# Optimization experiments

Measured on AMD Instinct MI355X. Metric: run time of the kernel, lower is better.

The kernel has to match this reference:

```python
import jax, jax.numpy as jnp
import numpy as np

B, N, C = 8, 2048, 512


def setup_inputs() -> dict:
    key = jax.random.key(0)
    ks = jax.random.split(key, 8)
    s = 1.0 / np.sqrt(C)
    return {
        "x": jax.random.normal(ks[0], (B, N, C), dtype=jnp.float32),
        "Wq": jax.random.normal(ks[1], (C, C), dtype=jnp.float32) * s,
        "Wk": jax.random.normal(ks[2], (C, C), dtype=jnp.float32) * s,
        "Wv": jax.random.normal(ks[3], (C, C), dtype=jnp.float32) * s,
        "W1": jax.random.normal(ks[4], (C, C), dtype=jnp.float32) * s,
        "W2": jax.random.normal(ks[5], (C, C), dtype=jnp.float32) * s,
        "gamma": jax.random.normal(ks[6], (1,), dtype=jnp.float32),
        "beta_p": jax.random.normal(ks[7], (1,), dtype=jnp.float32),
    }


def reference(x, Wq, Wk, Wv, W1, W2, gamma, beta_p):
    # torch.nn.Linear(bias=False): y = x @ W.T  with W of shape [out, in]
    q = jnp.einsum('bnc,dc->bnd', x, Wq)  # [B,N,C]
    k = jnp.einsum('bnc,dc->bnd', x, Wk)
    v = jnp.einsum('bnc,dc->bnd', x, Wv)
    # scores[b,i,j] = q_i . k_j ; softmax over dim=1 (the i axis), as in source
    scores = jnp.einsum('bic,bjc->bij', q, k)        # [B,N,N]
    attn = jax.nn.softmax(scores, axis=1)            # normalize over i
    # bmm(v^T, attn): out[b,c,j] = sum_i v[b,i,c] * attn[b,i,j]; permuted back -> [B,N,C]
    att_out = jnp.einsum('bic,bij->bjc', v, attn)    # [B,N,C]
    o = gamma * att_out + x                          # gamma-scaled residual
    h = jax.nn.relu(jnp.einsum('bnc,dc->bnd', o, W1))
    o = beta_p * jnp.einsum('bnc,dc->bnd', h, W2) + o
    return o
```

## Files before the change

kernel.cpp:

```cpp
#include <hip/hip_runtime.h>
#include <stdint.h>

#define DEVINL __device__ __forceinline__

typedef short short8_t __attribute__((ext_vector_type(8)));
typedef float f32x4_t  __attribute__((ext_vector_type(4)));
typedef _Float16 half8_t __attribute__((ext_vector_type(8)));
typedef unsigned short u16;

static constexpr int  Bn = 8;
static constexpr int  Nn = 2048;
static constexpr int  Cn = 512;
static constexpr int  Mn = Bn * Nn;
static constexpr long NC = (long)Nn * Cn;
static constexpr long NNe = (long)Nn * Nn;
static constexpr long CC = (long)Cn * Cn;
static constexpr long MC = (long)Mn * Cn;

DEVINL u16 f32_to_f16(float f) {
  _Float16 h = (_Float16)f;
  u16 r; __builtin_memcpy(&r, &h, 2);
  return r;
}

DEVINL void mfma_f16(f32x4_t& d, short8_t a, short8_t b) {
  asm("v_mfma_f32_16x16x32_f16 %0, %1, %2, %0" : "+v"(d) : "v"(a), "v"(b));
}

#define GLOAD_LDS16(G, L)                                                      \
  __builtin_amdgcn_global_load_lds(                                            \
      (const __attribute__((address_space(1))) void*)(G),                      \
      (__attribute__((address_space(3))) void*)(L), 16, 0, 0)

__global__ __launch_bounds__(256) void conv_x_kernel(const float* __restrict__ src,
                                                     u16* __restrict__ f16, int n4) {
  int i = blockIdx.x * 256 + threadIdx.x;
  if (i >= n4) return;
  float4 v = ((const float4*)src)[i];
  ((ushort4*)f16)[i] = make_ushort4(f32_to_f16(v.x), f32_to_f16(v.y),
                                    f32_to_f16(v.z), f32_to_f16(v.w));
}

struct W5 { const float* p[5]; };
__global__ __launch_bounds__(256) void conv_w_kernel(W5 ws, u16* __restrict__ f16,
                                                     int n4each) {
  const int w = blockIdx.y;
  const int i = blockIdx.x * 256 + threadIdx.x;
  if (i >= n4each) return;
  float4 v = ((const float4*)ws.p[w])[i];
  ((ushort4*)f16)[(long)w * (CC / 4) + i] =
      make_ushort4(f32_to_f16(v.x), f32_to_f16(v.y), f32_to_f16(v.z), f32_to_f16(v.w));
}

enum { EPI_QKV = 0, EPI_SF16 = 2, EPI_PV = 3, EPI_RELU = 4, EPI_FFN2 = 5 };

template <int BN, int EPI, int SW>
__global__ __launch_bounds__(512, 2) void gemm_k(
    const u16* Ah, const u16* Bh,
    int K, int outld, void* out0, void* out1,
    const float* aux, const float* scal,
    int batch0, long azStride, long bzStride, long ozStride) {
  constexpr int BM = 256, BK = 64;
  constexpr int FN = BN / 64;
  constexpr int ABYTES = BM * BK * 2;
  constexpr int BBYTES = BN * BK * 2;
  constexpr int PB = ABYTES + BBYTES;

  __shared__ __align__(1024) char lds[2 * PB];

  const int tid = threadIdx.x;
  const int l   = tid & 63;
  const int wid = tid >> 6;

  int bx, byy, bz;
  {
    const int gx = gridDim.x, gy = gridDim.y, gz = gridDim.z;
    const int lid = blockIdx.x + gx * (blockIdx.y + gy * blockIdx.z);
    if (SW == 0) {
      const int c = lid & 7, s = lid >> 3;
      const int nyz = gy * gz;
      const int xi = s / nyz, yz = s - xi * nyz;
      bx = c + 8 * xi; byy = yz % gy; bz = yz / gy;
    } else if (SW == 1) {
      bz = lid & 7;
      const int s = lid >> 3;
      byy = s % gy; bx = s / gy;
    } else {
      bx = blockIdx.x; byy = blockIdx.y; bz = blockIdx.z;
    }
  }

  const int batch = batch0 + bz;
  const int brow  = bx * BM;
  const int bcol  = byy * BN;

  Ah += (long)bz * azStride;
  Bh += (long)bz * bzStride;

  const int wrL  = (wid >> 2) * 128;
  const int wcL  = (wid & 3) * (BN / 4);
  const int rsel = l & 15;

  f32x4_t acc[8][FN];
  const f32x4_t zero = {0.f, 0.f, 0.f, 0.f};
#pragma unroll
  for (int m = 0; m < 8; ++m)
#pragma unroll
    for (int n = 0; n < FN; ++n) acc[m][n] = zero;

  const int cb = ((l & 7) ^ ((l >> 3) & 7)) * 8;
  auto stageA = [&](int k0, char* dst) {
#pragma unroll
    for (int j = 0; j < 4; ++j) {
      const int rr = (wid * 4 + j) * 8 + (l >> 3);
      GLOAD_LDS16(Ah + (long)(brow + rr) * K + (k0 + cb), dst + (wid * 4 + j) * 1024);
    }
  };
  auto stageB = [&](int k0, char* dst) {
#pragma unroll
    for (int j = 0; j < FN; ++j) {
      const int rr = (wid * FN + j) * 8 + (l >> 3);
      GLOAD_LDS16(Bh + (long)(bcol + rr) * K + (k0 + cb), dst + (wid * FN + j) * 1024);
    }
  };
  auto stageAll = [&](int k0, char* b) { stageA(k0, b); stageB(k0, b + ABYTES); };

  auto rdA = [&](const char* bufA, int m, int ks) -> short8_t {
    const int r = wrL + m * 16 + rsel;
    const int s = ks * 4 + (l >> 4);
    return *(const short8_t*)(bufA + r * 128 + ((s ^ (r & 7)) << 4));
  };
  auto rdB = [&](const char* bufB, int n, int ks) -> short8_t {
    const int r = wcL + n * 16 + rsel;
    const int s = ks * 4 + (l >> 4);
    return *(const short8_t*)(bufB + r * 128 + ((s ^ (r & 7)) << 4));
  };

  const int NT = K >> 6;
  stageAll(0, lds);
  for (int kt = 0; kt < NT; ++kt) {
    const char* bb = lds + (kt & 1) * PB;
    if (kt + 1 < NT) {
      stageAll((kt + 1) << 6, lds + ((kt + 1) & 1) * PB);
      __builtin_amdgcn_sched_barrier(0);
      if constexpr (FN == 2)
        asm volatile("s_waitcnt vmcnt(6)" ::: "memory");
      else
        asm volatile("s_waitcnt vmcnt(8)" ::: "memory");
    } else {
      __builtin_amdgcn_sched_barrier(0);
      asm volatile("s_waitcnt vmcnt(0)" ::: "memory");
    }
    __builtin_amdgcn_sched_barrier(0);
    __builtin_amdgcn_s_barrier();
    asm volatile("" ::: "memory");
    __builtin_amdgcn_sched_barrier(0);

    short8_t bf[FN][2];
#pragma unroll
    for (int n = 0; n < FN; ++n)
#pragma unroll
      for (int ks = 0; ks < 2; ++ks) bf[n][ks] = rdB(bb + ABYTES, n, ks);

    __builtin_amdgcn_s_setprio(1);
#pragma unroll
    for (int p = 0; p < 4; ++p) {
      short8_t a[2][2];
#pragma unroll
      for (int mm = 0; mm < 2; ++mm)
#pragma unroll
        for (int ks = 0; ks < 2; ++ks) a[mm][ks] = rdA(bb, 2 * p + mm, ks);
#pragma unroll
      for (int mm = 0; mm < 2; ++mm)
#pragma unroll
        for (int n = 0; n < FN; ++n)
#pragma unroll
          for (int ks = 0; ks < 2; ++ks)
            mfma_f16(acc[2 * p + mm][n], a[mm][ks], bf[n][ks]);
    }
    __builtin_amdgcn_s_setprio(0);

    __builtin_amdgcn_sched_barrier(0);
    asm volatile("" ::: "memory");
    __builtin_amdgcn_s_barrier();
    __builtin_amdgcn_sched_barrier(0);
  }

  const float sc0 = scal ? scal[0] : 0.0f;
  const int crow = (l >> 4) * 4;
  const int ccol = l & 15;

  if (EPI == EPI_QKV && (bcol >> 9) == 2) {
    constexpr int TP2 = 264;
    u16* t = (u16*)lds;
#pragma unroll
    for (int m = 0; m < 8; ++m)
#pragma unroll
      for (int n = 0; n < FN; ++n) {
        ushort4 pk = make_ushort4(f32_to_f16(acc[m][n][0]), f32_to_f16(acc[m][n][1]),
                                  f32_to_f16(acc[m][n][2]), f32_to_f16(acc[m][n][3]));
        *(ushort4*)&t[(wcL + n * 16 + ccol) * TP2 + (wrL + m * 16 + crow)] = pk;
      }
    __syncthreads();
    const int colq = tid >> 2, qf = tid & 3;
    const long b = brow >> 11;
    const int cv = bcol - 1024 + colq;
    u16* dst = (u16*)out1 + ((b * Cn + cv) * (long)Nn + (brow & 2047) + qf * 64);
    const u16* srcT = &t[colq * TP2 + qf * 64];
#pragma unroll
    for (int i = 0; i < 8; ++i)
      ((uint4*)dst)[i] = *(const uint4*)(srcT + i * 8);
    return;
  }

#pragma unroll
  for (int m = 0; m < 8; ++m)
#pragma unroll
    for (int n = 0; n < FN; ++n)
#pragma unroll
      for (int j = 0; j < 4; ++j) {
        const int r = brow + wrL + m * 16 + crow + j;
        const int c = bcol + wcL + n * 16 + ccol;
        const float v = acc[m][n][j];
        if (EPI == EPI_QKV) {
          ((u16*)out0)[(long)(c >> 9) * MC + (long)r * Cn + (c & 511)] = f32_to_f16(v);
        } else if (EPI == EPI_SF16) {
          ((u16*)out0 + (long)bz * ozStride)[(long)r * outld + c] = f32_to_f16(v);
        } else if (EPI == EPI_PV) {
          const long gi = ((long)batch * Nn + r) * Cn + c;
          const float val = sc0 * v + aux[gi];
          ((float*)out0)[gi] = val;
          ((u16*)out1)[gi] = f32_to_f16(val);
        } else if (EPI == EPI_RELU) {
          const float val = v > 0.f ? v : 0.f;
          ((u16*)out0)[(long)r * outld + c] = f32_to_f16(val);
        } else {
          const long gi = (long)r * Cn + c;
          ((float*)out0)[gi] = sc0 * v + aux[gi];
        }
      }
}

__global__ __launch_bounds__(256) void softmax_k(const u16* sc, u16* attn) {
  const long base = (long)blockIdx.y * NNe + (long)blockIdx.x * Nn;
  const int tid = threadIdx.x;
  const int l = tid & 63, wid = tid >> 6;
  half8_t v = ((const half8_t*)(sc + base))[tid];
  float f[8];
#pragma unroll
  for (int i = 0; i < 8; ++i) f[i] = (float)v[i];
  float mx = f[0];
#pragma unroll
  for (int i = 1; i < 8; ++i) mx = fmaxf(mx, f[i]);
#pragma unroll
  for (int o = 32; o > 0; o >>= 1) mx = fmaxf(mx, __shfl_xor(mx, o));
  __shared__ float red[8];
  if (l == 0) red[wid] = mx;
  __syncthreads();
  mx = fmaxf(fmaxf(red[0], red[1]), fmaxf(red[2], red[3]));
  float p[8];
  float s = 0.f;
#pragma unroll
  for (int i = 0; i < 8; ++i) { p[i] = __expf(f[i] - mx); s += p[i]; }
#pragma unroll
  for (int o = 32; o > 0; o >>= 1) s += __shfl_xor(s, o);
  if (l == 0) red[4 + wid] = s;
  __syncthreads();
  s = red[4] + red[5] + red[6] + red[7];
  const float inv = 1.0f / s;
  __align__(16) u16 o8[8];
#pragma unroll
  for (int i = 0; i < 8; ++i) o8[i] = f32_to_f16(p[i] * inv);
  ((uint4*)(attn + base))[tid] = *(const uint4*)o8;
}

extern "C" void kernel_launch(void* const* d_in, const int* in_sizes, int n_in,
                              void* d_out, int out_size, void* d_ws, size_t ws_size,
                              hipStream_t stream) {
  const float* x  = (const float*)d_in[0];
  const float* gamma = (const float*)d_in[6];
  const float* beta  = (const float*)d_in[7];
  float* out = (float*)d_out;

  char* ws = (char*)d_ws;
  size_t off = 0;
  auto alloc = [&](size_t bytes) {
    char* p = ws + off;
    off += (bytes + 1023) & ~(size_t)1023;
    return p;
  };
  u16* x16  = (u16*)alloc((size_t)MC * 2);
  u16* w16A = (u16*)alloc((size_t)5 * CC * 2);
  u16* qk16 = (u16*)alloc((size_t)2 * MC * 2);
  u16* vT   = (u16*)alloc((size_t)MC * 2);
  u16* o16  = (u16*)alloc((size_t)MC * 2);
  u16* h16  = (u16*)alloc((size_t)MC * 2);
  const size_t baseOff = off;

  int zAtt = 8;
  while (zAtt > 1 &&
         baseOff + (size_t)zAtt * (NNe * 2 + 1024 + NNe * 2 + 1024) > ws_size)
    zAtt >>= 1;
  u16* scoresT = (u16*)alloc((size_t)zAtt * NNe * 2);
  u16* attnT   = (u16*)alloc((size_t)zAtt * NNe * 2);
  u16* q16 = qk16;
  u16* k16 = qk16 + (size_t)MC;

  conv_x_kernel<<<dim3(MC / 4 / 256), 256, 0, stream>>>(x, x16, MC / 4);
  W5 w5 = {{(const float*)d_in[1], (const float*)d_in[2], (const float*)d_in[3],
            (const float*)d_in[4], (const float*)d_in[5]}};
  conv_w_kernel<<<dim3(CC / 4 / 256, 5), 256, 0, stream>>>(w5, w16A, CC / 4);

  gemm_k<128,EPI_QKV,0><<<dim3(Mn/256, 1536/128, 1), 512, 0, stream>>>(
      x16, w16A, Cn, Cn, qk16, vT, nullptr, nullptr, 0, 0, 0, 0);

  if (zAtt == 8) {
    gemm_k<256,EPI_SF16,1><<<dim3(Nn/256, Nn/256, 8), 512, 0, stream>>>(
        k16, q16, Cn, Nn, scoresT, nullptr, nullptr, nullptr, 0, NC, NC, NNe);
    softmax_k<<<dim3(Nn, 8), 256, 0, stream>>>(scoresT, attnT);
    gemm_k<128,EPI_PV,1><<<dim3(Nn/256, Cn/128, 8), 512, 0, stream>>>(
        attnT, vT, Nn, Cn, out, o16, x, gamma, 0, NNe, NC, 0);
  } else {
    for (int b0 = 0; b0 < Bn; b0 += zAtt) {
      gemm_k<256,EPI_SF16,2><<<dim3(Nn/256, Nn/256, zAtt), 512, 0, stream>>>(
          k16 + (long)b0 * NC, q16 + (long)b0 * NC,
          Cn, Nn, scoresT, nullptr, nullptr, nullptr, b0, NC, NC, NNe);
      softmax_k<<<dim3(Nn, zAtt), 256, 0, stream>>>(scoresT, attnT);
      gemm_k<128,EPI_PV,2><<<dim3(Nn/256, Cn/128, zAtt), 512, 0, stream>>>(
          attnT, vT + (long)b0 * NC, Nn, Cn, out, o16, x, gamma,
          b0, NNe, NC, 0);
    }
  }

  gemm_k<128,EPI_RELU,0><<<dim3(Mn/256, Cn/128, 1), 512, 0, stream>>>(
      o16, w16A + 3 * CC, Cn, Cn, h16, nullptr, nullptr, nullptr, 0, 0, 0, 0);
  gemm_k<128,EPI_FFN2,0><<<dim3(Mn/256, Cn/128, 1), 512, 0, stream>>>(
      h16, w16A + 4 * CC, Cn, Cn, out, nullptr, out, beta, 0, 0, 0, 0);
}
```

Baseline: 232.0 us.

## Rework GEMM warp tiling to 4 N-fragments and widen QKV tile to 256

Each wave now always computes 4 N-fragments, with the M-fragment count varying by tile width (8 for BN=256, 4 for BN=128). BN=128 kernels use a 4x2 wave grid of 64x64 subtiles instead of 2x4 of 128x32. The QKV projection launches with BN=256 tiles, and its transposed V epilogue runs in two passes through LDS. The aim is better operand reuse per A fragment and fewer QKV blocks, at the cost of more accumulator registers and an extra LDS pass with barriers in the V epilogue.

```diff
diff --git a/kernel.cpp b/kernel.cpp
--- a/kernel.cpp
+++ b/kernel.cpp
@@ -61,7 +61,9 @@
     const float* aux, const float* scal,
     int batch0, long azStride, long bzStride, long ozStride) {
   constexpr int BM = 256, BK = 64;
-  constexpr int FN = BN / 64;
+  constexpr int FM = (BN == 256) ? 8 : 4;
+  constexpr int FN = 4;
+  constexpr int BISS = BN / 64;
   constexpr int ABYTES = BM * BK * 2;
   constexpr int BBYTES = BN * BK * 2;
   constexpr int PB = ABYTES + BBYTES;
@@ -97,14 +99,14 @@
   Ah += (long)bz * azStride;
   Bh += (long)bz * bzStride;
 
-  const int wrL  = (wid >> 2) * 128;
-  const int wcL  = (wid & 3) * (BN / 4);
+  const int wrL  = (BN == 256) ? (wid >> 2) * 128 : (wid >> 1) * 64;
+  const int wcL  = (BN == 256) ? (wid & 3) * 64   : (wid & 1) * 64;
   const int rsel = l & 15;
 
-  f32x4_t acc[8][FN];
+  f32x4_t acc[FM][FN];
   const f32x4_t zero = {0.f, 0.f, 0.f, 0.f};
 #pragma unroll
-  for (int m = 0; m < 8; ++m)
+  for (int m = 0; m < FM; ++m)
 #pragma unroll
     for (int n = 0; n < FN; ++n) acc[m][n] = zero;
 
@@ -118,9 +120,9 @@
   };
   auto stageB = [&](int k0, char* dst) {
 #pragma unroll
-    for (int j = 0; j < FN; ++j) {
-      const int rr = (wid * FN + j) * 8 + (l >> 3);
-      GLOAD_LDS16(Bh + (long)(bcol + rr) * K + (k0 + cb), dst + (wid * FN + j) * 1024);
+    for (int j = 0; j < BISS; ++j) {
+      const int rr = (wid * BISS + j) * 8 + (l >> 3);
+      GLOAD_LDS16(Bh + (long)(bcol + rr) * K + (k0 + cb), dst + (wid * BISS + j) * 1024);
     }
   };
   auto stageAll = [&](int k0, char* b) { stageA(k0, b); stageB(k0, b + ABYTES); };
@@ -143,10 +145,10 @@
     if (kt + 1 < NT) {
       stageAll((kt + 1) << 6, lds + ((kt + 1) & 1) * PB);
       __builtin_amdgcn_sched_barrier(0);
-      if constexpr (FN == 2)
+      if constexpr (BN == 256)
+        asm volatile("s_waitcnt vmcnt(8)" ::: "memory");
+      else
         asm volatile("s_waitcnt vmcnt(6)" ::: "memory");
-      else
-        asm volatile("s_waitcnt vmcnt(8)" ::: "memory");
     } else {
       __builtin_amdgcn_sched_barrier(0);
       asm volatile("s_waitcnt vmcnt(0)" ::: "memory");
@@ -164,19 +166,14 @@
 
     __builtin_amdgcn_s_setprio(1);
 #pragma unroll
-    for (int p = 0; p < 4; ++p) {
-      short8_t a[2][2];
-#pragma unroll
-      for (int mm = 0; mm < 2; ++mm)
-#pragma unroll
-        for (int ks = 0; ks < 2; ++ks) a[mm][ks] = rdA(bb, 2 * p + mm, ks);
-#pragma unroll
-      for (int mm = 0; mm < 2; ++mm)
-#pragma unroll
-        for (int n = 0; n < FN; ++n)
-#pragma unroll
-          for (int ks = 0; ks < 2; ++ks)
-            mfma_f16(acc[2 * p + mm][n], a[mm][ks], bf[n][ks]);
+    for (int m = 0; m < FM; ++m) {
+      short8_t a0 = rdA(bb, m, 0);
+      short8_t a1 = rdA(bb, m, 1);
+#pragma unroll
+      for (int n = 0; n < FN; ++n) {
+        mfma_f16(acc[m][n], a0, bf[n][0]);
+        mfma_f16(acc[m][n], a1, bf[n][1]);
+      }
     }
     __builtin_amdgcn_s_setprio(0);
 
@@ -190,31 +187,39 @@
   const int crow = (l >> 4) * 4;
   const int ccol = l & 15;
 
-  if (EPI == EPI_QKV && (bcol >> 9) == 2) {
-    constexpr int TP2 = 264;
+  if (EPI == EPI_QKV && bcol >= 1024) {
+    constexpr int TPV = 264;
     u16* t = (u16*)lds;
-#pragma unroll
-    for (int m = 0; m < 8; ++m)
-#pragma unroll
-      for (int n = 0; n < FN; ++n) {
-        ushort4 pk = make_ushort4(f32_to_f16(acc[m][n][0]), f32_to_f16(acc[m][n][1]),
-                                  f32_to_f16(acc[m][n][2]), f32_to_f16(acc[m][n][3]));
-        *(ushort4*)&t[(wcL + n * 16 + ccol) * TP2 + (wrL + m * 16 + crow)] = pk;
+    const long b = brow >> 11;
+#pragma unroll
+    for (int pass = 0; pass < 2; ++pass) {
+      __syncthreads();
+      if (((wid & 3) >> 1) == pass) {
+        const int clBase = wcL - pass * 128;
+#pragma unroll
+        for (int m = 0; m < FM; ++m)
+#pragma unroll
+          for (int n = 0; n < FN; ++n) {
+            ushort4 pk = make_ushort4(
+                f32_to_f16(acc[m][n][0]), f32_to_f16(acc[m][n][1]),
+                f32_to_f16(acc[m][n][2]), f32_to_f16(acc[m][n][3]));
+            *(ushort4*)&t[(clBase + n * 16 + ccol) * TPV + (wrL + m * 16 + crow)] = pk;
+          }
       }
-    __syncthreads();
-    const int colq = tid >> 2, qf = tid & 3;
-    const long b = brow >> 11;
-    const int cv = bcol - 1024 + colq;
-    u16* dst = (u16*)out1 + ((b * Cn + cv) * (long)Nn + (brow & 2047) + qf * 64);
-    const u16* srcT = &t[colq * TP2 + qf * 64];
-#pragma unroll
-    for (int i = 0; i < 8; ++i)
-      ((uint4*)dst)[i] = *(const uint4*)(srcT + i * 8);
+      __syncthreads();
+      const int colq = tid >> 2, qf = tid & 3;
+      const int cv = bcol - 1024 + pass * 128 + colq;
+      u16* dst = (u16*)out1 + ((b * Cn + cv) * (long)Nn + (brow & 2047) + qf * 64);
+      const u16* srcT = &t[colq * TPV + qf * 64];
+#pragma unroll
+      for (int i = 0; i < 8; ++i)
+        ((uint4*)dst)[i] = *(const uint4*)(srcT + i * 8);
+    }
     return;
   }
 
 #pragma unroll
-  for (int m = 0; m < 8; ++m)
+  for (int m = 0; m < FM; ++m)
 #pragma unroll
     for (int n = 0; n < FN; ++n)
 #pragma unroll
@@ -311,7 +316,7 @@
             (const float*)d_in[4], (const float*)d_in[5]}};
   conv_w_kernel<<<dim3(CC / 4 / 256, 5), 256, 0, stream>>>(w5, w16A, CC / 4);
 
-  gemm_k<128,EPI_QKV,0><<<dim3(Mn/256, 1536/128, 1), 512, 0, stream>>>(
+  gemm_k<256,EPI_QKV,0><<<dim3(Mn/256, 1536/256, 1), 512, 0, stream>>>(
       x16, w16A, Cn, Cn, qk16, vT, nullptr, nullptr, 0, 0, 0, 0);
 
   if (zAtt == 8) {
```

New measurement: 233.3 us. About the same (+0.6%).
